# Kernel optimization log

Hardware: AMD Instinct MI355X
Metric: run time of the kernel (lower is better)

## Reference

```python
import jax, jax.numpy as jnp
import numpy as np

N, F = 2048, 128
HEADS, OUT_DIM = 8, 8
ALPHA = 0.2  # tf.nn.leaky_relu default


def setup_inputs() -> dict:
    key = jax.random.key(0)
    k1, k2, k3, k4 = jax.random.split(key, 4)
    X = jax.random.normal(k1, (N, F), dtype=jnp.float32)
    A = jax.random.randint(k2, (N, N), 0, 2, dtype=jnp.int32)
    W = jax.random.normal(k3, (F, OUT_DIM * HEADS), dtype=jnp.float32) * (1.0 / np.sqrt(F))
    attn_kernel = jax.random.normal(k4, (2 * OUT_DIM, 1), dtype=jnp.float32) * 0.1
    return {"X": X, "A": A, "W": W, "attn_kernel": attn_kernel}


def reference(X, A, W, attn_kernel):
    # h: [N, heads, out_dim]
    h = (X @ W).reshape(N, HEADS, OUT_DIM)
    # tensordot(concat(h_i, h_j), a) == h_i @ a1 + h_j @ a2 (linear before leaky_relu),
    # so avoid materializing the [N,N,heads,2*out_dim] tile-concat tensor.
    a1 = attn_kernel[:OUT_DIM, 0]
    a2 = attn_kernel[OUT_DIM:, 0]
    s1 = jnp.einsum('nhd,d->nh', h, a1)  # [N, heads]
    s2 = jnp.einsum('nhd,d->nh', h, a2)  # [N, heads]
    e = jax.nn.leaky_relu(s1[:, None, :] + s2[None, :, :], ALPHA)  # [N, N, heads]
    mask = (A > 0).astype(e.dtype)[:, :, None]
    e = e * mask - 1e9 * (1.0 - mask)
    attention = jax.nn.softmax(e, axis=1)  # softmax over neighbor axis (axis=1), as in source
    # Faithful to source: einsum 'nij,njh->nih' contracts the HEAD axis
    # (attention [N,N,heads] with h [N,heads,out_dim]) -> [N, N, out_dim]
    h_prime = jnp.einsum('nij,njh->nih', attention, h)
    h_prime = h_prime.reshape(-1, OUT_DIM * HEADS)  # [N*N/heads, out_dim*heads]
    return jax.nn.leaky_relu(h_prime, ALPHA)
```

## Files before the change

### kernel.cpp

```cpp
#include <hip/hip_runtime.h>
#include <hip/hip_bf16.h>

#define NN      2048
#define FDIM    128
#define HEADS   8
#define ODIM    8
#define HID     64
#define ALPHA   0.2f
#define TB      512
#define JPT     4

__device__ __forceinline__ float lrelu(float x) {
    return x > 0.f ? x : ALPHA * x;
}

__global__ __launch_bounds__(64) void gat_prep(
        const float* __restrict__ X,
        const float* __restrict__ W,
        const float* __restrict__ ak,
        float* __restrict__ H,
        float* __restrict__ S1,
        float* __restrict__ S2) {
    const int n = blockIdx.x;
    const int t = threadIdx.x;

    __shared__ float Xs[FDIM];
    __shared__ float hs[HID];

    Xs[t]      = X[(size_t)n * FDIM + t];
    Xs[t + 64] = X[(size_t)n * FDIM + 64 + t];
    __syncthreads();

    float acc = 0.f;
    #pragma unroll 8
    for (int k = 0; k < FDIM; ++k)
        acc = fmaf(Xs[k], W[k * HID + t], acc);

    H[(size_t)n * HID + t] = acc;
    hs[t] = acc;
    __syncthreads();

    if (t < 16) {
        const int head = t & 7;
        const float* a = ak + ((t < 8) ? 0 : ODIM);
        float s = 0.f;
        #pragma unroll
        for (int d = 0; d < ODIM; ++d)
            s = fmaf(hs[head * ODIM + d], a[d], s);
        if (t < 8) S1[n * HEADS + head] = s;
        else       S2[n * HEADS + head] = s;
    }
}

__global__ __launch_bounds__(TB) void gat_attn(
        const int*   __restrict__ A,
        const float* __restrict__ H,
        const float* __restrict__ S1,
        const float* __restrict__ S2,
        float* __restrict__ out) {
    const int i    = blockIdx.x;
    const int t    = threadIdx.x;
    const int wave = t >> 6;
    const int lane = t & 63;

    __shared__ int   As[NN];
    __shared__ float redM[8 * HEADS];
    __shared__ float redL[8 * HEADS];
    __shared__ float hhS[HID];

    const int4* Arow4 = (const int4*)(A + (size_t)i * NN);
    ((int4*)As)[t] = Arow4[t];

    float s1r[HEADS];
    #pragma unroll
    for (int h = 0; h < HEADS; ++h) s1r[h] = S1[i * HEADS + h];

    __syncthreads();

    float ev[JPT][HEADS];
    float mloc[HEADS];
    #pragma unroll
    for (int h = 0; h < HEADS; ++h) mloc[h] = -3.0e38f;

    #pragma unroll
    for (int jj = 0; jj < JPT; ++jj) {
        const int j = t + jj * TB;
        const float4 s2a = *(const float4*)(S2 + j * HEADS);
        const float4 s2b = *(const float4*)(S2 + j * HEADS + 4);
        const bool msk = As[j] > 0;
        const float s2v[8] = {s2a.x, s2a.y, s2a.z, s2a.w,
                              s2b.x, s2b.y, s2b.z, s2b.w};
        #pragma unroll
        for (int h = 0; h < HEADS; ++h) {
            const float x = s1r[h] + s2v[h];
            const float e = msk ? lrelu(x) : -1.0e9f;
            ev[jj][h] = e;
            mloc[h] = fmaxf(mloc[h], e);
        }
    }

    #pragma unroll
    for (int h = 0; h < HEADS; ++h) {
        float v = mloc[h];
        #pragma unroll
        for (int off = 32; off; off >>= 1)
            v = fmaxf(v, __shfl_xor(v, off));
        if (lane == 0) redM[wave * HEADS + h] = v;
    }
    __syncthreads();
    float mf[HEADS];
    #pragma unroll
    for (int h = 0; h < HEADS; ++h) {
        float v = redM[h];
        #pragma unroll
        for (int w = 1; w < 8; ++w)
            v = fmaxf(v, redM[w * HEADS + h]);
        mf[h] = v;
    }

    float ls[HEADS];
    #pragma unroll
    for (int h = 0; h < HEADS; ++h) ls[h] = 0.f;
    #pragma unroll
    for (int jj = 0; jj < JPT; ++jj) {
        #pragma unroll
        for (int h = 0; h < HEADS; ++h) {
            const float p = __expf(ev[jj][h] - mf[h]);
            ev[jj][h] = p;
            ls[h] += p;
        }
    }

    #pragma unroll
    for (int h = 0; h < HEADS; ++h) {
        float v = ls[h];
        #pragma unroll
        for (int off = 32; off; off >>= 1)
            v += __shfl_xor(v, off);
        if (lane == 0) redL[wave * HEADS + h] = v;
    }
    __syncthreads();
    float lf[HEADS];
    #pragma unroll
    for (int h = 0; h < HEADS; ++h) {
        float v = redL[h];
        #pragma unroll
        for (int w = 1; w < 8; ++w)
            v += redL[w * HEADS + h];
        lf[h] = v;
    }

    if (t < HID)
        hhS[t] = H[(size_t)i * HID + t] / lf[t >> 3];
    __syncthreads();

    float oacc[JPT][ODIM];
    #pragma unroll
    for (int jj = 0; jj < JPT; ++jj)
        #pragma unroll
        for (int d = 0; d < ODIM; ++d)
            oacc[jj][d] = 0.f;

    #pragma unroll
    for (int h = 0; h < HEADS; ++h) {
        const float4 h0 = *(const float4*)(hhS + h * ODIM);
        const float4 h1 = *(const float4*)(hhS + h * ODIM + 4);
        #pragma unroll
        for (int jj = 0; jj < JPT; ++jj) {
            const float p = ev[jj][h];
            oacc[jj][0] = fmaf(p, h0.x, oacc[jj][0]);
            oacc[jj][1] = fmaf(p, h0.y, oacc[jj][1]);
            oacc[jj][2] = fmaf(p, h0.z, oacc[jj][2]);
            oacc[jj][3] = fmaf(p, h0.w, oacc[jj][3]);
            oacc[jj][4] = fmaf(p, h1.x, oacc[jj][4]);
            oacc[jj][5] = fmaf(p, h1.y, oacc[jj][5]);
            oacc[jj][6] = fmaf(p, h1.z, oacc[jj][6]);
            oacc[jj][7] = fmaf(p, h1.w, oacc[jj][7]);
        }
    }

    #pragma unroll
    for (int jj = 0; jj < JPT; ++jj) {
        const int j = t + jj * TB;
        const size_t base = ((size_t)i * NN + j) * ODIM;
        float4 o0, o1;
        o0.x = lrelu(oacc[jj][0]); o0.y = lrelu(oacc[jj][1]);
        o0.z = lrelu(oacc[jj][2]); o0.w = lrelu(oacc[jj][3]);
        o1.x = lrelu(oacc[jj][4]); o1.y = lrelu(oacc[jj][5]);
        o1.z = lrelu(oacc[jj][6]); o1.w = lrelu(oacc[jj][7]);
        *(float4*)(out + base)     = o0;
        *(float4*)(out + base + 4) = o1;
    }
}

extern "C" void kernel_launch(void* const* d_in, const int* in_sizes, int n_in,
                              void* d_out, int out_size, void* d_ws, size_t ws_size,
                              hipStream_t stream) {
    const float* X  = (const float*)d_in[0];
    const int*   A  = (const int*)  d_in[1];
    const float* W  = (const float*)d_in[2];
    const float* ak = (const float*)d_in[3];
    float* out = (float*)d_out;

    float* H  = (float*)d_ws;
    float* S1 = H  + (size_t)NN * HID;
    float* S2 = S1 + (size_t)NN * HEADS;

    gat_prep<<<NN, 64, 0, stream>>>(X, W, ak, H, S1, S2);
    gat_attn<<<NN, TB, 0, stream>>>(A, H, S1, S2, out);
}
```

Measured before the change: 212.9 us.

## Split attention into row-sum and write kernels, drop max subtraction

Splits the fused attention kernel into a row-sum kernel that accumulates the softmax denominators per head and a write kernel that recomputes the exponentials and writes output. Max subtraction is removed and unnormalized exp is used directly, which frees the per-thread score array and a block reduction. The write kernel runs with 256 threads and an occupancy hint so more blocks can stay resident while streaming the large output. The risks are recomputing exp and rereading A in both kernels, an extra launch, and overflow in exp if scores grow large.

```diff
diff --git a/kernel.cpp b/kernel.cpp
--- a/kernel.cpp
+++ b/kernel.cpp
@@ -7,8 +7,6 @@
 #define ODIM    8
 #define HID     64
 #define ALPHA   0.2f
-#define TB      512
-#define JPT     4
 
 __device__ __forceinline__ float lrelu(float x) {
     return x > 0.f ? x : ALPHA * x;
@@ -52,21 +50,18 @@
     }
 }
 
-__global__ __launch_bounds__(TB) void gat_attn(
+__global__ __launch_bounds__(512) void gat_rowsum(
         const int*   __restrict__ A,
-        const float* __restrict__ H,
         const float* __restrict__ S1,
         const float* __restrict__ S2,
-        float* __restrict__ out) {
+        float* __restrict__ LF) {
     const int i    = blockIdx.x;
     const int t    = threadIdx.x;
     const int wave = t >> 6;
     const int lane = t & 63;
 
     __shared__ int   As[NN];
-    __shared__ float redM[8 * HEADS];
     __shared__ float redL[8 * HEADS];
-    __shared__ float hhS[HID];
 
     const int4* Arow4 = (const int4*)(A + (size_t)i * NN);
     ((int4*)As)[t] = Arow4[t];
@@ -77,14 +72,13 @@
 
     __syncthreads();
 
-    float ev[JPT][HEADS];
-    float mloc[HEADS];
-    #pragma unroll
-    for (int h = 0; h < HEADS; ++h) mloc[h] = -3.0e38f;
-
-    #pragma unroll
-    for (int jj = 0; jj < JPT; ++jj) {
-        const int j = t + jj * TB;
+    float ls[HEADS];
+    #pragma unroll
+    for (int h = 0; h < HEADS; ++h) ls[h] = 0.f;
+
+    #pragma unroll
+    for (int jj = 0; jj < 4; ++jj) {
+        const int j = t + jj * 512;
         const float4 s2a = *(const float4*)(S2 + j * HEADS);
         const float4 s2b = *(const float4*)(S2 + j * HEADS + 4);
         const bool msk = As[j] > 0;
@@ -93,41 +87,7 @@
         #pragma unroll
         for (int h = 0; h < HEADS; ++h) {
             const float x = s1r[h] + s2v[h];
-            const float e = msk ? lrelu(x) : -1.0e9f;
-            ev[jj][h] = e;
-            mloc[h] = fmaxf(mloc[h], e);
-        }
-    }
-
-    #pragma unroll
-    for (int h = 0; h < HEADS; ++h) {
-        float v = mloc[h];
-        #pragma unroll
-        for (int off = 32; off; off >>= 1)
-            v = fmaxf(v, __shfl_xor(v, off));
-        if (lane == 0) redM[wave * HEADS + h] = v;
-    }
-    __syncthreads();
-    float mf[HEADS];
-    #pragma unroll
-    for (int h = 0; h < HEADS; ++h) {
-        float v = redM[h];
-        #pragma unroll
-        for (int w = 1; w < 8; ++w)
-            v = fmaxf(v, redM[w * HEADS + h]);
-        mf[h] = v;
-    }
-
-    float ls[HEADS];
-    #pragma unroll
-    for (int h = 0; h < HEADS; ++h) ls[h] = 0.f;
-    #pragma unroll
-    for (int jj = 0; jj < JPT; ++jj) {
-        #pragma unroll
-        for (int h = 0; h < HEADS; ++h) {
-            const float p = __expf(ev[jj][h] - mf[h]);
-            ev[jj][h] = p;
-            ls[h] += p;
+            ls[h] += msk ? __expf(lrelu(x)) : 0.f;
         }
     }
 
@@ -140,54 +100,81 @@
         if (lane == 0) redL[wave * HEADS + h] = v;
     }
     __syncthreads();
-    float lf[HEADS];
-    #pragma unroll
-    for (int h = 0; h < HEADS; ++h) {
-        float v = redL[h];
-        #pragma unroll
-        for (int w = 1; w < 8; ++w)
-            v += redL[w * HEADS + h];
-        lf[h] = v;
-    }
+
+    if (t < HEADS) {
+        float v = 0.f;
+        #pragma unroll
+        for (int w = 0; w < 8; ++w)
+            v += redL[w * HEADS + t];
+        LF[i * HEADS + t] = v;
+    }
+}
+
+__global__ __launch_bounds__(256, 4) void gat_write(
+        const int*   __restrict__ A,
+        const float* __restrict__ H,
+        const float* __restrict__ S1,
+        const float* __restrict__ S2,
+        const float* __restrict__ LF,
+        float* __restrict__ out) {
+    const int i = blockIdx.x;
+    const int t = threadIdx.x;
+
+    __shared__ int   As[NN];
+    __shared__ float hhS[HID];
+
+    const int4* Arow4 = (const int4*)(A + (size_t)i * NN);
+    ((int4*)As)[t]       = Arow4[t];
+    ((int4*)As)[t + 256] = Arow4[t + 256];
 
     if (t < HID)
-        hhS[t] = H[(size_t)i * HID + t] / lf[t >> 3];
-    __syncthreads();
-
-    float oacc[JPT][ODIM];
-    #pragma unroll
-    for (int jj = 0; jj < JPT; ++jj)
-        #pragma unroll
-        for (int d = 0; d < ODIM; ++d)
-            oacc[jj][d] = 0.f;
-
-    #pragma unroll
-    for (int h = 0; h < HEADS; ++h) {
-        const float4 h0 = *(const float4*)(hhS + h * ODIM);
-        const float4 h1 = *(const float4*)(hhS + h * ODIM + 4);
-        #pragma unroll
-        for (int jj = 0; jj < JPT; ++jj) {
-            const float p = ev[jj][h];
-            oacc[jj][0] = fmaf(p, h0.x, oacc[jj][0]);
-            oacc[jj][1] = fmaf(p, h0.y, oacc[jj][1]);
-            oacc[jj][2] = fmaf(p, h0.z, oacc[jj][2]);
-            oacc[jj][3] = fmaf(p, h0.w, oacc[jj][3]);
-            oacc[jj][4] = fmaf(p, h1.x, oacc[jj][4]);
-            oacc[jj][5] = fmaf(p, h1.y, oacc[jj][5]);
-            oacc[jj][6] = fmaf(p, h1.z, oacc[jj][6]);
-            oacc[jj][7] = fmaf(p, h1.w, oacc[jj][7]);
+        hhS[t] = H[(size_t)i * HID + t] / LF[i * HEADS + (t >> 3)];
+
+    float s1r[HEADS];
+    #pragma unroll
+    for (int h = 0; h < HEADS; ++h) s1r[h] = S1[i * HEADS + h];
+
+    __syncthreads();
+
+    float hh[HID];
+    #pragma unroll
+    for (int k = 0; k < HID; k += 4) {
+        const float4 v = *(const float4*)(hhS + k);
+        hh[k] = v.x; hh[k + 1] = v.y; hh[k + 2] = v.z; hh[k + 3] = v.w;
+    }
+
+    #pragma unroll
+    for (int jj = 0; jj < 8; ++jj) {
+        const int j = t + jj * 256;
+        const float4 s2a = *(const float4*)(S2 + j * HEADS);
+        const float4 s2b = *(const float4*)(S2 + j * HEADS + 4);
+        const bool msk = As[j] > 0;
+        const float s2v[8] = {s2a.x, s2a.y, s2a.z, s2a.w,
+                              s2b.x, s2b.y, s2b.z, s2b.w};
+
+        float p[HEADS];
+        #pragma unroll
+        for (int h = 0; h < HEADS; ++h) {
+            const float x = s1r[h] + s2v[h];
+            p[h] = msk ? __expf(lrelu(x)) : 0.f;
         }
-    }
-
-    #pragma unroll
-    for (int jj = 0; jj < JPT; ++jj) {
-        const int j = t + jj * TB;
+
+        float o[ODIM];
+        #pragma unroll
+        for (int d = 0; d < ODIM; ++d) o[d] = 0.f;
+        #pragma unroll
+        for (int h = 0; h < HEADS; ++h) {
+            #pragma unroll
+            for (int d = 0; d < ODIM; ++d)
+                o[d] = fmaf(p[h], hh[h * ODIM + d], o[d]);
+        }
+
         const size_t base = ((size_t)i * NN + j) * ODIM;
         float4 o0, o1;
-        o0.x = lrelu(oacc[jj][0]); o0.y = lrelu(oacc[jj][1]);
-        o0.z = lrelu(oacc[jj][2]); o0.w = lrelu(oacc[jj][3]);
-        o1.x = lrelu(oacc[jj][4]); o1.y = lrelu(oacc[jj][5]);
-        o1.z = lrelu(oacc[jj][6]); o1.w = lrelu(oacc[jj][7]);
+        o0.x = lrelu(o[0]); o0.y = lrelu(o[1]);
+        o0.z = lrelu(o[2]); o0.w = lrelu(o[3]);
+        o1.x = lrelu(o[4]); o1.y = lrelu(o[5]);
+        o1.z = lrelu(o[6]); o1.w = lrelu(o[7]);
         *(float4*)(out + base)     = o0;
         *(float4*)(out + base + 4) = o1;
     }
@@ -205,7 +192,9 @@
     float* H  = (float*)d_ws;
     float* S1 = H  + (size_t)NN * HID;
     float* S2 = S1 + (size_t)NN * HEADS;
-
-    gat_prep<<<NN, 64, 0, stream>>>(X, W, ak, H, S1, S2);
-    gat_attn<<<NN, TB, 0, stream>>>(A, H, S1, S2, out);
-}
+    float* LF = S2 + (size_t)NN * HEADS;
+
+    gat_prep  <<<NN,  64, 0, stream>>>(X, W, ak, H, S1, S2);
+    gat_rowsum<<<NN, 512, 0, stream>>>(A, S1, S2, LF);
+    gat_write <<<NN, 256, 0, stream>>>(A, H, S1, S2, LF, out);
+}
```

New measurement: 179.0 us. -15.9%, faster.
